# Kernel optimization log

Hardware: AMD Instinct MI355X
Metric: run time of the kernel (lower is better)

The kernel has to match this reference:

```python
import jax, jax.numpy as jnp
import numpy as np

EMBED = 1024
NUM_EXPERTS = 8
TOP_K = 2


def setup_inputs() -> dict:
    key = jax.random.key(0)
    ks = jax.random.split(key, 6)
    scale = EMBED ** -0.5  # keep activations numerically sane
    return {
        "x": jax.random.normal(ks[0], (4, 4096, EMBED), jnp.float32),
        "router_w": jax.random.normal(ks[1], (EMBED, NUM_EXPERTS), jnp.float32) * scale,
        "router_b": jnp.zeros((NUM_EXPERTS,), jnp.float32),
        "we_gate": jax.random.normal(ks[2], (NUM_EXPERTS, EMBED, EMBED), jnp.float32) * scale,
        "we_up": jax.random.normal(ks[3], (NUM_EXPERTS, EMBED, EMBED), jnp.float32) * scale,
        "we_down": jax.random.normal(ks[4], (NUM_EXPERTS, EMBED, EMBED), jnp.float32) * scale,
    }


def reference(x, router_w, router_b, we_gate, we_up, we_down):
    x_shape = x.shape
    x_flat = x.reshape(-1, x_shape[-1])            # [T, D]
    num_tokens = x_flat.shape[0]

    router_logits = x_flat @ router_w + router_b    # [T, E]
    topk_weights, topk_indices = jax.lax.top_k(router_logits, k=TOP_K)
    topk_weights = jax.nn.softmax(topk_weights, axis=-1)  # [T, K]

    token_idx_mesh = jnp.repeat(jnp.arange(num_tokens), TOP_K)  # [T*K]
    expert_idx_mesh = topk_indices.reshape(-1)                  # [T*K]

    sort_permutation = jnp.argsort(expert_idx_mesh)  # stable sort by expert
    sorted_expert_idx = expert_idx_mesh[sort_permutation]
    sorted_token_idx = token_idx_mesh[sort_permutation]
    group_sizes = jnp.bincount(sorted_expert_idx, length=NUM_EXPERTS)

    sorted_tokens = x_flat[sorted_token_idx]  # [T*K, D] gather (ragged dispatch)

    ff_gate = jax.lax.ragged_dot(sorted_tokens, we_gate, group_sizes)  # [T*K, D]
    ff_up = jax.lax.ragged_dot(sorted_tokens, we_up, group_sizes)      # [T*K, D]
    activated = jax.nn.silu(ff_gate) * ff_up
    ff_out = jax.lax.ragged_dot(activated, we_down, group_sizes)       # [T*K, D]

    # fuse router weighting into the combine (scatter-add) step
    sorted_weights = topk_weights.reshape(-1)[sort_permutation]  # [T*K]
    ff_out = ff_out * sorted_weights[:, None]

    output_flat = jnp.zeros_like(x_flat).at[sorted_token_idx].add(ff_out)
    return output_flat.reshape(x_shape)
```

## Files before the change

kernel.cpp:

```cpp
#include <hip/hip_runtime.h>
#include <hip/hip_bf16.h>
#include <cstdint>
#include <cstddef>

typedef unsigned short u16;
typedef unsigned int u32;
typedef __attribute__((ext_vector_type(8))) short short8;
typedef __attribute__((ext_vector_type(4))) float floatx4;

#define DD 1024
#define NE 8

#define GLOAD_LDS16(G, L)                                               \
  __builtin_amdgcn_global_load_lds(                                     \
      (const __attribute__((address_space(1))) void*)(G),               \
      (__attribute__((address_space(3))) void*)(L), 16, 0, 0)

#define LDSA(P) ((u32)(uintptr_t)(const __attribute__((address_space(3))) void*)(P))

#define DSR(DST, ADDR, IMM)                                             \
  asm volatile("ds_read_b128 %0, %1 offset:" IMM : "=v"(DST) : "v"(ADDR))

__device__ __forceinline__ u16 f2bf(float f) {
  union { __hip_bfloat16 h; u16 u; } cv;
  cv.h = __float2bfloat16(f);
  return cv.u;
}

__device__ __forceinline__ float2 bf2f2(u32 u) {
  union { u32 v; float f; } lo, hi;
  lo.v = u << 16; hi.v = u & 0xffff0000u;
  float2 r; r.x = lo.f; r.y = hi.f; return r;
}

__global__ __launch_bounds__(256) void router_kernel(
    const float* __restrict__ x, const float* __restrict__ rw,
    const float* __restrict__ rb, int2* __restrict__ experts,
    float2* __restrict__ wts, u16* __restrict__ xbf, int T) {
  const int wave = threadIdx.x >> 6;
  const int lane = threadIdx.x & 63;
  const int t = blockIdx.x * 4 + wave;
  if (t >= T) return;
  const float* xr = x + (size_t)t * DD;
  float acc[NE] = {0.f, 0.f, 0.f, 0.f, 0.f, 0.f, 0.f, 0.f};
#pragma unroll
  for (int i = 0; i < 16; i++) {
    const int idx = lane + i * 64;
    const float xv = xr[idx];
    xbf[(size_t)t * DD + idx] = f2bf(xv);
    const float4* r4 = (const float4*)(rw + (size_t)idx * NE);
    float4 a = r4[0], b = r4[1];
    acc[0] += xv * a.x; acc[1] += xv * a.y; acc[2] += xv * a.z; acc[3] += xv * a.w;
    acc[4] += xv * b.x; acc[5] += xv * b.y; acc[6] += xv * b.z; acc[7] += xv * b.w;
  }
#pragma unroll
  for (int s = 1; s < 64; s <<= 1)
#pragma unroll
    for (int e = 0; e < NE; e++)
      acc[e] += __shfl_xor(acc[e], s);
  if (lane == 0) {
    float lg[NE];
#pragma unroll
    for (int e = 0; e < NE; e++) lg[e] = acc[e] + rb[e];
    float l0 = lg[0]; int i0 = 0;
#pragma unroll
    for (int e = 1; e < NE; e++) if (lg[e] > l0) { l0 = lg[e]; i0 = e; }
    float l1 = -3.4e38f; int i1 = 0;
#pragma unroll
    for (int e = 0; e < NE; e++) {
      if (e == i0) continue;
      if (lg[e] > l1) { l1 = lg[e]; i1 = e; }
    }
    const float w0 = 1.f / (1.f + expf(l1 - l0));
    experts[t] = make_int2(i0, i1);
    wts[t] = make_float2(w0, 1.f - w0);
  }
}

__global__ __launch_bounds__(256) void count_kernel(
    const int2* __restrict__ experts, int* __restrict__ counts, int T) {
  __shared__ int lc[NE];
  if (threadIdx.x < NE) lc[threadIdx.x] = 0;
  __syncthreads();
  const int t = blockIdx.x * 256 + threadIdx.x;
  if (t < T) {
    int2 e = experts[t];
    atomicAdd(&lc[e.x], 1);
    atomicAdd(&lc[e.y], 1);
  }
  __syncthreads();
  if (threadIdx.x < NE && lc[threadIdx.x] > 0)
    atomicAdd(&counts[threadIdx.x], lc[threadIdx.x]);
}

__global__ void offsets_kernel(const int* __restrict__ counts, int* __restrict__ offsets) {
  int s = 0;
  for (int e = 0; e < NE; e++) { offsets[e] = s; s += counts[e]; }
}

__global__ __launch_bounds__(256) void scatter_kernel(
    const int2* __restrict__ experts, const int* __restrict__ offsets,
    int* __restrict__ cursors, int* __restrict__ tok_id,
    int2* __restrict__ slots, int T) {
  __shared__ int lc[NE], lb[NE];
  if (threadIdx.x < NE) lc[threadIdx.x] = 0;
  __syncthreads();
  const int t = blockIdx.x * 256 + threadIdx.x;
  int2 e = make_int2(0, 0);
  int p0 = 0, p1 = 0;
  if (t < T) {
    e = experts[t];
    p0 = atomicAdd(&lc[e.x], 1);
    p1 = atomicAdd(&lc[e.y], 1);
  }
  __syncthreads();
  if (threadIdx.x < NE) lb[threadIdx.x] = atomicAdd(&cursors[threadIdx.x], lc[threadIdx.x]);
  __syncthreads();
  if (t < T) {
    const int s0 = offsets[e.x] + lb[e.x] + p0;
    const int s1 = offsets[e.y] + lb[e.y] + p1;
    tok_id[s0] = t;
    tok_id[s1] = t;
    slots[t] = make_int2(s0, s1);
  }
}

__global__ __launch_bounds__(256) void convert_kernel(
    const float* __restrict__ wg, const float* __restrict__ wu,
    const float* __restrict__ wd, u16* __restrict__ Wgu, u16* __restrict__ Wd) {
  const int z = blockIdx.z;
  const int mat = z >> 3;
  const int e = z & 7;
  const float* src = (mat == 0 ? wg : (mat == 1 ? wu : wd)) + (size_t)e * DD * DD;
  __shared__ float tile[64][65];
  const int k0 = blockIdx.y * 64, n0 = blockIdx.x * 64;
  const int tx = threadIdx.x & 63, ty = threadIdx.x >> 6;
#pragma unroll
  for (int i = 0; i < 16; i++) {
    const int kk = i * 4 + ty;
    tile[kk][tx] = src[(size_t)(k0 + kk) * DD + n0 + tx];
  }
  __syncthreads();
#pragma unroll
  for (int i = 0; i < 16; i++) {
    const int nn = i * 4 + ty;
    const int n = n0 + nn;
    const u16 h = f2bf(tile[tx][nn]);
    if (mat == 2) {
      Wd[((size_t)e * DD + n) * DD + k0 + tx] = h;
    } else {
      const int nc = ((n >> 3) << 4) | (mat << 3) | (n & 7);
      Wgu[((size_t)e * 2048 + nc) * DD + k0 + tx] = h;
    }
  }
}


#define COMPUTE(BUFOB, DO_STAGE, SBUF)                                  \
  {                                                                     \
    short8 a[8], b[4];                                                  \
    const u32 ab_ = asb + (u32)(BUFOB) + offAB;                         \
    const u32 bb_ = bsb + (u32)(BUFOB) + offBB;                         \
    DSR(a[0], ab_, "0");    DSR(a[1], ab_, "1024");                     \
    DSR(a[2], ab_, "2048"); DSR(a[3], ab_, "3072");                     \
    DSR(a[4], ab_, "4096"); DSR(a[5], ab_, "5120");                     \
    DSR(a[6], ab_, "6144"); DSR(a[7], ab_, "7168");                     \
    DSR(b[0], bb_, "0");    DSR(b[1], bb_, "1024");                     \
    DSR(b[2], bb_, "2048"); DSR(b[3], bb_, "3072");                     \
    if (DO_STAGE) {                                                     \
      GLOAD_LDS16(sA0, &As[(SBUF) * 8192 + t * 8]);                     \
      GLOAD_LDS16(sA1, &As[(SBUF) * 8192 + 4096 + t * 8]);              \
      GLOAD_LDS16(sB0, &Bs[(SBUF) * 8192 + t * 8]);                     \
      GLOAD_LDS16(sB1, &Bs[(SBUF) * 8192 + 4096 + t * 8]);              \
      sA0 += 32; sA1 += 32; sB0 += 32; sB1 += 32;                       \
    }                                                                   \
    asm volatile("s_waitcnt lgkmcnt(0)");                               \
    __builtin_amdgcn_sched_barrier(0);                                  \
    __builtin_amdgcn_s_setprio(1);                                      \
    _Pragma("unroll")                                                   \
    for (int i = 0; i < 8; i++)                                         \
      _Pragma("unroll")                                                 \
      for (int j = 0; j < 4; j++)                                       \
        acc[i][j] = __builtin_amdgcn_mfma_f32_16x16x32_bf16(            \
            a[i], b[j], acc[i][j], 0, 0, 0);                            \
    __builtin_amdgcn_s_setprio(0);                                      \
    __builtin_amdgcn_sched_barrier(0);                                  \
  }

#define STAGE(BUF)                                                      \
  {                                                                     \
    GLOAD_LDS16(sA0, &As[(BUF) * 8192 + t * 8]);                        \
    GLOAD_LDS16(sA1, &As[(BUF) * 8192 + 4096 + t * 8]);                 \
    GLOAD_LDS16(sB0, &Bs[(BUF) * 8192 + t * 8]);                        \
    GLOAD_LDS16(sB1, &Bs[(BUF) * 8192 + 4096 + t * 8]);                 \
    sA0 += 32; sA1 += 32; sB0 += 32; sB1 += 32;                         \
  }

#define SYNC(VM)                                                        \
  __builtin_amdgcn_sched_barrier(0);                                    \
  asm volatile("s_waitcnt vmcnt(" VM ")");                              \
  __builtin_amdgcn_s_barrier();                                         \
  __builtin_amdgcn_sched_barrier(0);

#define GEMM256_LOOP()                                                  \
  STAGE(0); STAGE(1); STAGE(2);                                         \
  SYNC("8");                                                            \
  _Pragma("unroll 1")                                                   \
  for (int kt = 0; kt < 29; ++kt) {                                     \
    COMPUTE((kt & 3) * 16384, 1, (kt + 3) & 3);                         \
    SYNC("8");                                                          \
  }                                                                     \
  COMPUTE(1 * 16384, 0, 0);                                             \
  SYNC("4");                                                            \
  COMPUTE(2 * 16384, 0, 0);                                             \
  SYNC("0");                                                            \
  COMPUTE(3 * 16384, 0, 0);

__global__ __launch_bounds__(512, 2) void gateup_kernel(
    const u16* __restrict__ xbf, const u16* __restrict__ Wgu,
    const int* __restrict__ tok_id, const int* __restrict__ offsets,
    const int* __restrict__ counts, u16* __restrict__ H) {
  const int e = blockIdx.z;
  const int cnt = counts[e];
  const int m0 = blockIdx.y * 256;
  if (m0 >= cnt) return;
  const int off = offsets[e];
  const int n0 = blockIdx.x * 256;

  __shared__ u16 As[4 * 8192];
  __shared__ u16 Bs[4 * 8192];

  const int t = threadIdx.x;
  const int lane = t & 63;
  const int wave = t >> 6;
  const int wm = (wave >> 2) * 128;
  const int wn = (wave & 3) * 64;
  const int r16 = lane & 15;
  const int quad = lane >> 4;
  const int swz = quad ^ ((r16 >> 1) & 3);
  const u32 offAB = (u32)((wm + r16) * 64 + swz * 16);
  const u32 offBB = (u32)((wn + r16) * 64 + swz * 16);
  const u32 asb = LDSA(&As[0]);
  const u32 bsb = LDSA(&Bs[0]);

  const int drow = t >> 2;
  const int dpos = t & 3;
  const int c8 = (dpos ^ ((drow >> 1) & 3)) * 8;
  int r0 = m0 + drow;       if (r0 > cnt - 1) r0 = cnt - 1;
  int r1 = m0 + drow + 128; if (r1 > cnt - 1) r1 = cnt - 1;
  const u16* sA0 = xbf + (size_t)tok_id[off + r0] * DD + c8;
  const u16* sA1 = xbf + (size_t)tok_id[off + r1] * DD + c8;
  const u16* bbase = Wgu + ((size_t)e * 2048 + n0) * DD + c8;
  const u16* sB0 = bbase + (size_t)drow * DD;
  const u16* sB1 = bbase + (size_t)(drow + 128) * DD;

  floatx4 acc[8][4];
#pragma unroll
  for (int i = 0; i < 8; i++)
#pragma unroll
    for (int j = 0; j < 4; j++)
      acc[i][j] = (floatx4){0.f, 0.f, 0.f, 0.f};

  GEMM256_LOOP();

#pragma unroll
  for (int i = 0; i < 8; i++) {
    const int mb = m0 + wm + i * 16 + quad * 4;
#pragma unroll
    for (int j = 0; j < 4; j++) {
      const int nc = n0 + wn + j * 16 + r16;
      const int ng = ((nc >> 4) << 3) | (nc & 7);
#pragma unroll
      for (int r = 0; r < 4; r++) {
        const float v = acc[i][j][r];
        const float pv = __shfl_xor(v, 8);
        const float g = (lane & 8) ? pv : v;
        const float u = (lane & 8) ? v : pv;
        const float hv = g * u / (1.f + __expf(-g));
        const int m = mb + r;
        if (!(lane & 8) && m < cnt)
          H[(size_t)(off + m) * DD + ng] = f2bf(hv);
      }
    }
  }
}

__global__ __launch_bounds__(512, 2) void down_kernel(
    const u16* __restrict__ H, const u16* __restrict__ Wd,
    const int* __restrict__ counts, const int* __restrict__ offsets,
    u16* __restrict__ Y, int TK2) {
  const int e = blockIdx.z;
  const int cnt = counts[e];
  const int m0 = blockIdx.y * 256;
  if (m0 >= cnt) return;
  const int off = offsets[e];
  const int n0 = blockIdx.x * 256;

  __shared__ u16 As[4 * 8192];
  __shared__ u16 Bs[4 * 8192];

  const int t = threadIdx.x;
  const int lane = t & 63;
  const int wave = t >> 6;
  const int wm = (wave >> 2) * 128;
  const int wn = (wave & 3) * 64;
  const int r16 = lane & 15;
  const int quad = lane >> 4;
  const int swz = quad ^ ((r16 >> 1) & 3);
  const u32 offAB = (u32)((wm + r16) * 64 + swz * 16);
  const u32 offBB = (u32)((wn + r16) * 64 + swz * 16);
  const u32 asb = LDSA(&As[0]);
  const u32 bsb = LDSA(&Bs[0]);

  const int drow = t >> 2;
  const int dpos = t & 3;
  const int c8 = (dpos ^ ((drow >> 1) & 3)) * 8;
  int r0 = off + m0 + drow;       if (r0 > TK2 - 1) r0 = TK2 - 1;
  int r1 = off + m0 + drow + 128; if (r1 > TK2 - 1) r1 = TK2 - 1;
  const u16* sA0 = H + (size_t)r0 * DD + c8;
  const u16* sA1 = H + (size_t)r1 * DD + c8;
  const u16* bbase = Wd + ((size_t)e * DD + n0) * DD + c8;
  const u16* sB0 = bbase + (size_t)drow * DD;
  const u16* sB1 = bbase + (size_t)(drow + 128) * DD;

  floatx4 acc[8][4];
#pragma unroll
  for (int i = 0; i < 8; i++)
#pragma unroll
    for (int j = 0; j < 4; j++)
      acc[i][j] = (floatx4){0.f, 0.f, 0.f, 0.f};

  GEMM256_LOOP();

#pragma unroll
  for (int i = 0; i < 8; i++) {
    const int mb = m0 + wm + i * 16 + quad * 4;
#pragma unroll
    for (int r = 0; r < 4; r++) {
      const int m = mb + r;
      if (m < cnt) {
        u16* yrow = Y + (size_t)(off + m) * DD + n0 + wn + r16;
#pragma unroll
        for (int j = 0; j < 4; j++)
          yrow[j * 16] = f2bf(acc[i][j][r]);
      }
    }
  }
}

#undef STAGE
#undef COMPUTE
#undef SYNC

__global__ __launch_bounds__(256) void combine_kernel(
    const u16* __restrict__ Y, const int2* __restrict__ slots,
    const float2* __restrict__ wts, float* __restrict__ out, int T) {
  const int wave = threadIdx.x >> 6;
  const int lane = threadIdx.x & 63;
  const int t = blockIdx.x * 4 + wave;
  if (t >= T) return;
  const int2 s = slots[t];
  const float2 w = wts[t];
  const uint4* y0 = (const uint4*)(Y + (size_t)s.x * DD);
  const uint4* y1 = (const uint4*)(Y + (size_t)s.y * DD);
  float4* o = (float4*)(out + (size_t)t * DD);
#pragma unroll
  for (int c = 0; c < 2; c++) {
    const int idx = lane + c * 64;
    const uint4 a = y0[idx];
    const uint4 b = y1[idx];
    const u32 au[4] = {a.x, a.y, a.z, a.w};
    const u32 bu[4] = {b.x, b.y, b.z, b.w};
    float4 r[2];
#pragma unroll
    for (int q = 0; q < 4; q++) {
      const float2 fa = bf2f2(au[q]);
      const float2 fb = bf2f2(bu[q]);
      ((float*)r)[q * 2]     = w.x * fa.x + w.y * fb.x;
      ((float*)r)[q * 2 + 1] = w.x * fa.y + w.y * fb.y;
    }
    o[idx * 2]     = r[0];
    o[idx * 2 + 1] = r[1];
  }
}

extern "C" void kernel_launch(void* const* d_in, const int* in_sizes, int n_in,
                              void* d_out, int out_size, void* d_ws, size_t ws_size,
                              hipStream_t stream) {
  const float* x  = (const float*)d_in[0];
  const float* rw = (const float*)d_in[1];
  const float* rb = (const float*)d_in[2];
  const float* wg = (const float*)d_in[3];
  const float* wu = (const float*)d_in[4];
  const float* wd = (const float*)d_in[5];
  float* out = (float*)d_out;
  const int T = in_sizes[0] / DD;
  const int TK2 = 2 * T;

  char* p = (char*)d_ws;
  int* ctrl = (int*)p; p += 256;
  int2* experts = (int2*)p;  p += (size_t)T * 8;
  float2* wtsp  = (float2*)p; p += (size_t)T * 8;
  int* tok_id   = (int*)p;   p += (size_t)TK2 * 4;
  int2* slots   = (int2*)p;  p += (size_t)T * 8;
  u16* Wd       = (u16*)p;   p += (size_t)NE * DD * DD * 2;
  u16* H        = (u16*)p;   p += (size_t)TK2 * DD * 2;
  u16* Wgu      = (u16*)p;
  u16* xbf      = (u16*)(p + (size_t)NE * 2048 * DD * 2);
  u16* Y        = (u16*)p;
  p += (size_t)TK2 * DD * 2;
  if ((size_t)(p - (char*)d_ws) > ws_size) return;

  hipMemsetAsync(ctrl, 0, 256, stream);

  router_kernel<<<T / 4, 256, 0, stream>>>(x, rw, rb, experts, wtsp, xbf, T);
  count_kernel<<<T / 256, 256, 0, stream>>>(experts, ctrl, T);
  offsets_kernel<<<1, 1, 0, stream>>>(ctrl, ctrl + 16);
  scatter_kernel<<<T / 256, 256, 0, stream>>>(experts, ctrl + 16, ctrl + 8, tok_id, slots, T);
  convert_kernel<<<dim3(16, 16, 24), 256, 0, stream>>>(wg, wu, wd, Wgu, Wd);
  gateup_kernel<<<dim3(8, (T + 255) / 256, NE), 512, 0, stream>>>(
      xbf, Wgu, tok_id, ctrl + 16, ctrl, H);
  down_kernel<<<dim3(4, (T + 255) / 256, NE), 512, 0, stream>>>(
      H, Wd, ctrl, ctrl + 16, Y, TK2);
  combine_kernel<<<T / 4, 256, 0, stream>>>(Y, slots, wtsp, out, T);
}
```

Before: 519.9 us.

## Pre-tile weights and intermediate H into swizzled contiguous 128x32 blocks

Converts the expert weights (and the gate-up output H) into a blocked layout in which each 128-row by 32-k tile is stored contiguously with the LDS swizzle already applied. Each thread's global-to-LDS load then reads a fully contiguous 8KB chunk instead of 64-byte strided row pieces. The goal is better global memory coalescing and fewer DRAM/TLB pages touched per stage. Stage issue is also moved ahead of the LDS reads in COMPUTE. In exchange, H stores in the gate-up epilogue become more scattered, and the address math is more complex.

Measured after the change: 537.4 us. +3.4%, slower.

```diff
diff --git a/kernel.cpp b/kernel.cpp
--- a/kernel.cpp
+++ b/kernel.cpp
@@ -10,6 +10,7 @@
 
 #define DD 1024
 #define NE 8
+
 
 #define GLOAD_LDS16(G, L)                                               \
   __builtin_amdgcn_global_load_lds(                                     \
@@ -141,23 +142,39 @@
     tile[kk][tx] = src[(size_t)(k0 + kk) * DD + n0 + tx];
   }
   __syncthreads();
+  const int k = k0 + tx;
+  const int kt = k >> 5, c = (k >> 3) & 3, j8 = k & 7;
 #pragma unroll
   for (int i = 0; i < 16; i++) {
     const int nn = i * 4 + ty;
     const int n = n0 + nn;
     const u16 h = f2bf(tile[tx][nn]);
     if (mat == 2) {
-      Wd[((size_t)e * DD + n) * DD + k0 + tx] = h;
+      const int r = n & 127, nb = n >> 7;
+      const int pos = c ^ ((r >> 1) & 3);
+      Wd[((size_t)(e * 8 + nb) * 32 + kt) * 4096 + r * 32 + pos * 8 + j8] = h;
     } else {
       const int nc = ((n >> 3) << 4) | (mat << 3) | (n & 7);
-      Wgu[((size_t)e * 2048 + nc) * DD + k0 + tx] = h;
+      const int r = nc & 127, nb = nc >> 7;
+      const int pos = c ^ ((r >> 1) & 3);
+      Wgu[((size_t)(e * 16 + nb) * 32 + kt) * 4096 + r * 32 + pos * 8 + j8] = h;
     }
   }
 }
 
 
-#define COMPUTE(BUFOB, DO_STAGE, SBUF)                                  \
+#define STAGE(BUF, INCA)                                                \
   {                                                                     \
+    GLOAD_LDS16(sA0, &As[(BUF) * 8192 + t * 8]);                        \
+    GLOAD_LDS16(sA1, &As[(BUF) * 8192 + 4096 + t * 8]);                 \
+    GLOAD_LDS16(sB0, &Bs[(BUF) * 8192 + t * 8]);                        \
+    GLOAD_LDS16(sB1, &Bs[(BUF) * 8192 + 4096 + t * 8]);                 \
+    sA0 += (INCA); sA1 += (INCA); sB0 += 4096; sB1 += 4096;             \
+  }
+
+#define COMPUTE(BUFOB, DO_STAGE, SBUF, INCA)                            \
+  {                                                                     \
+    if (DO_STAGE) { STAGE(SBUF, INCA); }                                \
     short8 a[8], b[4];                                                  \
     const u32 ab_ = asb + (u32)(BUFOB) + offAB;                         \
     const u32 bb_ = bsb + (u32)(BUFOB) + offBB;                         \
@@ -167,13 +184,6 @@
     DSR(a[6], ab_, "6144"); DSR(a[7], ab_, "7168");                     \
     DSR(b[0], bb_, "0");    DSR(b[1], bb_, "1024");                     \
     DSR(b[2], bb_, "2048"); DSR(b[3], bb_, "3072");                     \
-    if (DO_STAGE) {                                                     \
-      GLOAD_LDS16(sA0, &As[(SBUF) * 8192 + t * 8]);                     \
-      GLOAD_LDS16(sA1, &As[(SBUF) * 8192 + 4096 + t * 8]);              \
-      GLOAD_LDS16(sB0, &Bs[(SBUF) * 8192 + t * 8]);                     \
-      GLOAD_LDS16(sB1, &Bs[(SBUF) * 8192 + 4096 + t * 8]);              \
-      sA0 += 32; sA1 += 32; sB0 += 32; sB1 += 32;                       \
-    }                                                                   \
     asm volatile("s_waitcnt lgkmcnt(0)");                               \
     __builtin_amdgcn_sched_barrier(0);                                  \
     __builtin_amdgcn_s_setprio(1);                                      \
@@ -187,34 +197,25 @@
     __builtin_amdgcn_sched_barrier(0);                                  \
   }
 
-#define STAGE(BUF)                                                      \
-  {                                                                     \
-    GLOAD_LDS16(sA0, &As[(BUF) * 8192 + t * 8]);                        \
-    GLOAD_LDS16(sA1, &As[(BUF) * 8192 + 4096 + t * 8]);                 \
-    GLOAD_LDS16(sB0, &Bs[(BUF) * 8192 + t * 8]);                        \
-    GLOAD_LDS16(sB1, &Bs[(BUF) * 8192 + 4096 + t * 8]);                 \
-    sA0 += 32; sA1 += 32; sB0 += 32; sB1 += 32;                         \
-  }
-
 #define SYNC(VM)                                                        \
   __builtin_amdgcn_sched_barrier(0);                                    \
   asm volatile("s_waitcnt vmcnt(" VM ")");                              \
   __builtin_amdgcn_s_barrier();                                         \
   __builtin_amdgcn_sched_barrier(0);
 
-#define GEMM256_LOOP()                                                  \
-  STAGE(0); STAGE(1); STAGE(2);                                         \
+#define GEMM256_LOOP(INCA)                                              \
+  STAGE(0, INCA); STAGE(1, INCA); STAGE(2, INCA);                       \
   SYNC("8");                                                            \
   _Pragma("unroll 1")                                                   \
   for (int kt = 0; kt < 29; ++kt) {                                     \
-    COMPUTE((kt & 3) * 16384, 1, (kt + 3) & 3);                         \
+    COMPUTE((kt & 3) * 16384, 1, (kt + 3) & 3, INCA);                   \
     SYNC("8");                                                          \
   }                                                                     \
-  COMPUTE(1 * 16384, 0, 0);                                             \
+  COMPUTE(1 * 16384, 0, 0, INCA);                                       \
   SYNC("4");                                                            \
-  COMPUTE(2 * 16384, 0, 0);                                             \
+  COMPUTE(2 * 16384, 0, 0, INCA);                                       \
   SYNC("0");                                                            \
-  COMPUTE(3 * 16384, 0, 0);
+  COMPUTE(3 * 16384, 0, 0, INCA);
 
 __global__ __launch_bounds__(512, 2) void gateup_kernel(
     const u16* __restrict__ xbf, const u16* __restrict__ Wgu,
@@ -244,15 +245,14 @@
   const u32 bsb = LDSA(&Bs[0]);
 
   const int drow = t >> 2;
-  const int dpos = t & 3;
-  const int c8 = (dpos ^ ((drow >> 1) & 3)) * 8;
+  const int pos = t & 3;
+  const int c8 = (pos ^ ((drow >> 1) & 3)) * 8;
   int r0 = m0 + drow;       if (r0 > cnt - 1) r0 = cnt - 1;
   int r1 = m0 + drow + 128; if (r1 > cnt - 1) r1 = cnt - 1;
   const u16* sA0 = xbf + (size_t)tok_id[off + r0] * DD + c8;
   const u16* sA1 = xbf + (size_t)tok_id[off + r1] * DD + c8;
-  const u16* bbase = Wgu + ((size_t)e * 2048 + n0) * DD + c8;
-  const u16* sB0 = bbase + (size_t)drow * DD;
-  const u16* sB1 = bbase + (size_t)(drow + 128) * DD;
+  const u16* sB0 = Wgu + (size_t)(e * 16 + (n0 >> 7)) * 131072 + t * 8;
+  const u16* sB1 = Wgu + (size_t)(e * 16 + (n0 >> 7) + 1) * 131072 + t * 8;
 
   floatx4 acc[8][4];
 #pragma unroll
@@ -261,7 +261,7 @@
     for (int j = 0; j < 4; j++)
       acc[i][j] = (floatx4){0.f, 0.f, 0.f, 0.f};
 
-  GEMM256_LOOP();
+  GEMM256_LOOP(32);
 
 #pragma unroll
   for (int i = 0; i < 8; i++) {
@@ -270,6 +270,7 @@
     for (int j = 0; j < 4; j++) {
       const int nc = n0 + wn + j * 16 + r16;
       const int ng = ((nc >> 4) << 3) | (nc & 7);
+      const int kt = ng >> 5, c = (ng >> 3) & 3, j8 = ng & 7;
 #pragma unroll
       for (int r = 0; r < 4; r++) {
         const float v = acc[i][j][r];
@@ -278,8 +279,12 @@
         const float u = (lane & 8) ? v : pv;
         const float hv = g * u / (1.f + __expf(-g));
         const int m = mb + r;
-        if (!(lane & 8) && m < cnt)
-          H[(size_t)(off + m) * DD + ng] = f2bf(hv);
+        if (!(lane & 8) && m < cnt) {
+          const int s = off + m;
+          const int rr = s & 127;
+          const int p2 = c ^ ((rr >> 1) & 3);
+          H[(size_t)(s >> 7) * 131072 + kt * 4096 + rr * 32 + p2 * 8 + j8] = f2bf(hv);
+        }
       }
     }
   }
@@ -313,15 +318,14 @@
   const u32 bsb = LDSA(&Bs[0]);
 
   const int drow = t >> 2;
-  const int dpos = t & 3;
-  const int c8 = (dpos ^ ((drow >> 1) & 3)) * 8;
-  int r0 = off + m0 + drow;       if (r0 > TK2 - 1) r0 = TK2 - 1;
-  int r1 = off + m0 + drow + 128; if (r1 > TK2 - 1) r1 = TK2 - 1;
-  const u16* sA0 = H + (size_t)r0 * DD + c8;
-  const u16* sA1 = H + (size_t)r1 * DD + c8;
-  const u16* bbase = Wd + ((size_t)e * DD + n0) * DD + c8;
-  const u16* sB0 = bbase + (size_t)drow * DD;
-  const u16* sB1 = bbase + (size_t)(drow + 128) * DD;
+  const int pos = t & 3;
+  const int c = pos ^ ((drow >> 1) & 3);
+  int s0 = off + m0 + drow;        if (s0 > TK2 - 1) s0 = TK2 - 1;
+  int s1 = off + m0 + drow + 128;  if (s1 > TK2 - 1) s1 = TK2 - 1;
+  const u16* sA0 = H + (size_t)(s0 >> 7) * 131072 + (s0 & 127) * 32 + (c ^ ((s0 >> 1) & 3)) * 8;
+  const u16* sA1 = H + (size_t)(s1 >> 7) * 131072 + (s1 & 127) * 32 + (c ^ ((s1 >> 1) & 3)) * 8;
+  const u16* sB0 = Wd + (size_t)(e * 8 + (n0 >> 7)) * 131072 + t * 8;
+  const u16* sB1 = Wd + (size_t)(e * 8 + (n0 >> 7) + 1) * 131072 + t * 8;
 
   floatx4 acc[8][4];
 #pragma unroll
@@ -330,7 +334,7 @@
     for (int j = 0; j < 4; j++)
       acc[i][j] = (floatx4){0.f, 0.f, 0.f, 0.f};
 
-  GEMM256_LOOP();
+  GEMM256_LOOP(4096);
 
 #pragma unroll
   for (int i = 0; i < 8; i++) {
```
